# Kernel tuning notes

Hardware: AMD Instinct MI355X
Metric: run time of the kernel (lower is better)

Reference implementation:

```python
import jax, jax.numpy as jnp
import numpy as np

EPS = 1e-5

def setup_inputs() -> dict:
    key = jax.random.key(0)
    ks = jax.random.split(key, 6)
    N, K, Cin, Cout = 40000, 27, 128, 128
    feats = jax.random.normal(ks[0], (N, Cin), dtype=jnp.float32)
    W = jax.random.normal(ks[1], (K, Cin, Cout), dtype=jnp.float32) * (1.0 / np.sqrt(Cin * K))
    gamma = jnp.ones((Cout,), dtype=jnp.float32)
    beta = jnp.zeros((Cout,), dtype=jnp.float32)
    in_idx = jax.random.randint(ks[2], (K, N), 0, N, dtype=jnp.int64)
    out_idx = jax.random.randint(ks[3], (K, N), 0, N, dtype=jnp.int64)
    valid = jax.random.randint(ks[4], (K, N), 0, 2, dtype=jnp.int32)
    return {"feats": feats, "W": W, "gamma": gamma, "beta": beta,
            "in_idx": in_idx, "out_idx": out_idx, "valid": valid}

def reference(feats, W, gamma, beta, in_idx, out_idx, valid) -> jnp.ndarray:
    # Sparse 3D conv as gather-GEMM-scatter over K=27 kernel-offset maps.
    K, M = in_idx.shape
    N = feats.shape[0]  # stride 1 -> N_out == N_in
    mask = (valid > 0).astype(feats.dtype)[..., None]          # [K, M, 1]
    gathered = feats[in_idx] * mask                            # [K, M, Cin]
    msg = jnp.einsum('kmc,kcd->kmd', gathered, W)              # [K, M, Cout]
    out = jax.ops.segment_sum(msg.reshape(K * M, -1),
                              out_idx.reshape(-1),
                              num_segments=N)                   # [N, Cout]
    # MinkowskiBatchNorm (training mode): batch stats over all active points.
    mean = jnp.mean(out, axis=0)
    var = jnp.var(out, axis=0)
    y = (out - mean) * jax.lax.rsqrt(var + EPS) * gamma + beta
    # MinkowskiGELU == exact (erf) GELU.
    return jax.nn.gelu(y, approximate=False)
```

## Files before the change

kernel.cpp:

```cpp
#include <hip/hip_runtime.h>

typedef unsigned short u16;
typedef unsigned int u32;
typedef unsigned long long u64;
using f32x4 = __attribute__((ext_vector_type(4))) float;
using bf16x8 = __attribute__((ext_vector_type(8))) short;

#define CIN 128
#define COUT 128
#define BM 128
#define LDA 136

__device__ inline u16 bf16rn(float f) {
    union { float f; u32 u; } v; v.f = f;
    u32 u = v.u;
    u += 0x7FFFu + ((u >> 16) & 1u);
    return (u16)(u >> 16);
}

__global__ void precast_feats_k(const float* __restrict__ in, u16* __restrict__ out, int total8) {
    int i = blockIdx.x * blockDim.x + threadIdx.x;
    if (i >= total8) return;
    const float4* p = (const float4*)in + 2 * (size_t)i;
    float4 a = p[0], b = p[1];
    u32 o0 = (u32)bf16rn(a.x) | ((u32)bf16rn(a.y) << 16);
    u32 o1 = (u32)bf16rn(a.z) | ((u32)bf16rn(a.w) << 16);
    u32 o2 = (u32)bf16rn(b.x) | ((u32)bf16rn(b.y) << 16);
    u32 o3 = (u32)bf16rn(b.z) | ((u32)bf16rn(b.w) << 16);
    ((uint4*)out)[i] = make_uint4(o0, o1, o2, o3);
}

__global__ void precast_w_k(const float* __restrict__ W, u16* __restrict__ Wt, int total) {
    int i = blockIdx.x * blockDim.x + threadIdx.x;
    if (i >= total) return;
    int k = i >> 14;
    int rem = i & 16383;
    int f = rem >> 9;
    int l = (rem >> 3) & 63;
    int e = rem & 7;
    int cn = f >> 2, kk = f & 3;
    int d = cn * 16 + (l & 15);
    int c = kk * 32 + ((l >> 4) << 3) + e;
    Wt[i] = bf16rn(W[(k << 14) + (c << 7) + d]);
}

__global__ void prep_k(const float* __restrict__ feats, const float* __restrict__ W,
                       const int* __restrict__ oi, const int* __restrict__ valid,
                       u16* __restrict__ fb, u16* __restrict__ Wt,
                       int* __restrict__ cnt, int* __restrict__ pos,
                       int* __restrict__ bc0, int* __restrict__ bc1,
                       int total8, int totalw, int N, int E, int b0, int b1) {
    const int blk = blockIdx.x;
    const int tid = threadIdx.x;
    if (blk < b0) {
        int i = blk * 256 + tid;
        if (i >= total8) return;
        const float4* p = (const float4*)feats + 2 * (size_t)i;
        float4 a = p[0], q = p[1];
        u32 o0 = (u32)bf16rn(a.x) | ((u32)bf16rn(a.y) << 16);
        u32 o1 = (u32)bf16rn(a.z) | ((u32)bf16rn(a.w) << 16);
        u32 o2 = (u32)bf16rn(q.x) | ((u32)bf16rn(q.y) << 16);
        u32 o3 = (u32)bf16rn(q.z) | ((u32)bf16rn(q.w) << 16);
        ((uint4*)fb)[i] = make_uint4(o0, o1, o2, o3);
    } else if (blk < b0 + b1) {
        int i = (blk - b0) * 256 + tid;
        if (i >= totalw) return;
        int k = i >> 14;
        int rem = i & 16383;
        int f = rem >> 9;
        int l = (rem >> 3) & 63;
        int e = rem & 7;
        int cn = f >> 2, kk = f & 3;
        int d = cn * 16 + (l & 15);
        int c = kk * 32 + ((l >> 4) << 3) + e;
        Wt[i] = bf16rn(W[(k << 14) + (c << 7) + d]);
    } else {
        const int b = blk - b0 - b1;
        const int e = b * 256 + tid;
        const int k0 = (b * 256) / N;
        bool v = false; bool g = false;
        if (e < E) {
            v = valid[e] > 0;
            g = (e >= (k0 + 1) * N);
            if (v) pos[e] = atomicAdd(&cnt[oi[e]], 1);
        }
        const int lane = tid & 63, wid = tid >> 6;
        u64 m0 = __ballot(v && !g);
        u64 m1 = __ballot(v && g);
        __shared__ int wt[4][2];
        if (lane == 0) { wt[wid][0] = __popcll(m0); wt[wid][1] = __popcll(m1); }
        __syncthreads();
        if (tid == 0) bc0[b] = wt[0][0] + wt[1][0] + wt[2][0] + wt[3][0];
        if (tid == 1) bc1[b] = wt[0][1] + wt[1][1] + wt[2][1] + wt[3][1];
    }
}

__global__ void hist_k(const int* __restrict__ oi, const int* __restrict__ valid,
                       int* __restrict__ cnt, int* __restrict__ pos,
                       int* __restrict__ bc0, int* __restrict__ bc1, int N, int E) {
    const int tid = threadIdx.x;
    const int b = blockIdx.x;
    const int e = b * 256 + tid;
    const int k0 = (b * 256) / N;
    bool v = false; bool g = false;
    if (e < E) {
        v = valid[e] > 0;
        g = (e >= (k0 + 1) * N);
        if (v) pos[e] = atomicAdd(&cnt[oi[e]], 1);
    }
    const int lane = tid & 63, wid = tid >> 6;
    u64 m0 = __ballot(v && !g);
    u64 m1 = __ballot(v && g);
    __shared__ int wt[4][2];
    if (lane == 0) { wt[wid][0] = __popcll(m0); wt[wid][1] = __popcll(m1); }
    __syncthreads();
    if (tid == 0) bc0[b] = wt[0][0] + wt[1][0] + wt[2][0] + wt[3][0];
    if (tid == 1) bc1[b] = wt[0][1] + wt[1][1] + wt[2][1] + wt[3][1];
}

__global__ void scan_sum_k(const int* __restrict__ cnt, int* __restrict__ bsum, int N) {
    __shared__ int red[256];
    int t = threadIdx.x;
    int i = blockIdx.x * 256 + t;
    red[t] = (i < N) ? cnt[i] : 0;
    __syncthreads();
    #pragma unroll
    for (int d = 128; d > 0; d >>= 1) {
        if (t < d) red[t] += red[t + d];
        __syncthreads();
    }
    if (t == 0) bsum[blockIdx.x] = red[0];
}

__global__ void scan_top_k(int* __restrict__ bsum, int nb) {
    __shared__ int part[1024];
    int t = threadIdx.x;
    int v = (t < nb) ? bsum[t] : 0;
    part[t] = v;
    __syncthreads();
    for (int d = 1; d < 1024; d <<= 1) {
        int x = (t >= d) ? part[t - d] : 0;
        __syncthreads();
        part[t] += x;
        __syncthreads();
    }
    if (t < nb) bsum[t] = part[t] - v;
}

__global__ void scan_apply_kscan_k(const int* __restrict__ cnt, const int* __restrict__ bsum,
                                   int* __restrict__ offs,
                                   const int* __restrict__ bc0, const int* __restrict__ bc1,
                                   int* __restrict__ base0, int* __restrict__ base1,
                                   int* __restrict__ kcount, int N, int nb) {
    const int t = threadIdx.x;
    __shared__ int part[256];
    if ((int)blockIdx.x < nb) {
        int i = blockIdx.x * 256 + t;
        int v = (i < N) ? cnt[i] : 0;
        part[t] = v;
        __syncthreads();
        #pragma unroll
        for (int d = 1; d < 256; d <<= 1) {
            int x = (t >= d) ? part[t - d] : 0;
            __syncthreads();
            part[t] += x;
            __syncthreads();
        }
        int base = bsum[blockIdx.x];
        if (i < N) {
            int excl = base + part[t] - v;
            offs[i] = excl;
            if (i == N - 1) offs[N] = excl + v;
        }
    } else {
        const int k = blockIdx.x - nb;
        const int blo = (k * N) / 256;
        const int bhi = ((k + 1) * N - 1) / 256;
        const int len = bhi - blo + 1;
        const int b = blo + t;
        int k0b = 0, contrib = 0;
        const bool inr = (t < len);
        if (inr) {
            k0b = (b * 256) / N;
            contrib = (k0b == k) ? bc0[b] : bc1[b];
        }
        part[t] = contrib;
        __syncthreads();
        #pragma unroll
        for (int d = 1; d < 256; d <<= 1) {
            int x = (t >= d) ? part[t - d] : 0;
            __syncthreads();
            part[t] += x;
            __syncthreads();
        }
        if (inr) {
            int excl = part[t] - contrib;
            if (k0b == k) base0[b] = excl; else base1[b] = excl;
            if (t == len - 1) kcount[k] = part[t];
        }
    }
}

__global__ void rank_k(const int* __restrict__ oi, const int* __restrict__ ini,
                       const int* __restrict__ valid, const int* __restrict__ pos,
                       const int* __restrict__ offs,
                       const int* __restrict__ base0, const int* __restrict__ base1,
                       int* __restrict__ cin_arr, int* __restrict__ cpos_arr,
                       int N, int E, int cap) {
    const int tid = threadIdx.x;
    const int b = blockIdx.x;
    const int e = b * 256 + tid;
    const int k0 = (b * 256) / N;
    bool v = false; int k = 0, n = 0, ii = 0, p = 0;
    if (e < E) {
        v = valid[e] > 0;
        k = (e >= (k0 + 1) * N) ? k0 + 1 : k0;
        if (v) { n = oi[e]; ii = ini[e]; p = pos[e]; }
    }
    const int g = k - k0;
    const int lane = tid & 63, wid = tid >> 6;
    u64 m0 = __ballot(v && g == 0);
    u64 m1 = __ballot(v && g == 1);
    u64 lt = (1ull << lane) - 1ull;
    int r0 = __popcll(m0 & lt);
    int r1 = __popcll(m1 & lt);
    __shared__ int wt[4][2];
    if (lane == 0) { wt[wid][0] = __popcll(m0); wt[wid][1] = __popcll(m1); }
    __syncthreads();
    if (v) {
        int wbase = 0;
        #pragma unroll
        for (int w2 = 0; w2 < 4; ++w2) if (w2 < wid) wbase += wt[w2][g];
        int kb = g ? base1[b] : base0[b];
        int slot = kb + wbase + (g ? r1 : r0);
        int pg = offs[n] + p;
        cin_arr[k * N + slot] = ii;
        cpos_arr[k * N + slot] = (pg < cap) ? pg : (cap + n);
    }
}

__launch_bounds__(512, 6)
__global__ void convA_k(const u16* __restrict__ fb, const u16* __restrict__ Wt,
                        const int* __restrict__ cin_arr, const int* __restrict__ cpos_arr,
                        const int* __restrict__ kcount, u32* __restrict__ msg,
                        float* __restrict__ out, int N, int cap)
{
    const int k = blockIdx.y;
    const int kc = kcount[k];
    const int m0 = blockIdx.x * BM;
    if (m0 >= kc) return;

    __shared__ __align__(16) u16 Bsub[COUT * CIN];

    const int tid = threadIdx.x;
    const int wave = tid >> 6, lane = tid & 63;
    const int l15 = lane & 15, l4 = lane >> 4;
    const int base = k * N;

    int r0 = m0 + wave * 16 + l15;
    int i0 = cin_arr[base + min(r0, kc - 1)];
    if (r0 >= kc) i0 = 0;
    const u16* pa0 = fb + (size_t)i0 * CIN + l4 * 8;
    bf16x8 a0[4];
    #pragma unroll
    for (int kk = 0; kk < 4; ++kk)
        a0[kk] = *(const bf16x8*)(pa0 + kk * 32);

    {
        const u16* wk = Wt + ((size_t)k << 14);
        #pragma unroll
        for (int j = 0; j < 4; ++j)
            *(uint4*)(Bsub + j * 4096 + tid * 8) = *(const uint4*)(wk + j * 4096 + tid * 8);
    }
    __syncthreads();

    f32x4 acc[8];
    #pragma unroll
    for (int y = 0; y < 8; ++y)
        acc[y] = (f32x4){0.f, 0.f, 0.f, 0.f};

    #pragma unroll
    for (int kk = 0; kk < 4; ++kk) {
        #pragma unroll
        for (int cn = 0; cn < 8; ++cn) {
            bf16x8 b = *(const bf16x8*)(Bsub + (((cn << 2) + kk) << 9) + lane * 8);
            acc[cn] = __builtin_amdgcn_mfma_f32_16x16x32_bf16(a0[kk], b, acc[cn], 0, 0, 0);
        }
    }

    #pragma unroll
    for (int j = 0; j < 4; ++j) {
        int rl = m0 + wave * 16 + l4 * 4 + j;
        if (rl >= kc) continue;
        int v = cpos_arr[base + rl];
        if (v < cap) {
            u32 w0 = (u32)bf16rn(acc[0][j]) | ((u32)bf16rn(acc[1][j]) << 16);
            u32 w1 = (u32)bf16rn(acc[2][j]) | ((u32)bf16rn(acc[3][j]) << 16);
            u32 w2 = (u32)bf16rn(acc[4][j]) | ((u32)bf16rn(acc[5][j]) << 16);
            u32 w3 = (u32)bf16rn(acc[6][j]) | ((u32)bf16rn(acc[7][j]) << 16);
            *(uint4*)(msg + (size_t)v * 64 + 4 * l15) = make_uint4(w0, w1, w2, w3);
        } else {
            int n = v - cap;
            float* dst = out + (size_t)n * COUT + l15;
            #pragma unroll
            for (int cn = 0; cn < 8; ++cn)
                atomicAdd(dst + cn * 16, acc[cn][j]);
        }
    }
}

__global__ void convB_stats_k(const u32* __restrict__ msg, const int* __restrict__ offs,
                              float* __restrict__ out, float* __restrict__ stats,
                              int N, int cap, int nblk)
{
    const int tid = threadIdx.x;
    const int wave = tid >> 6, lane = tid & 63;
    const int sub = lane >> 4, l15 = lane & 15;
    const int colA = l15 + 32 * sub;
    float sA = 0.f, qA = 0.f, sB = 0.f, qB = 0.f;

    for (int n = blockIdx.x * 4 + wave; n < N; n += nblk * 4) {
        int s = min(offs[n], cap), e = min(offs[n + 1], cap);
        float a0 = 0.f, a1 = 0.f, a2 = 0.f, a3 = 0.f;
        float b0 = 0.f, b1 = 0.f, b2 = 0.f, b3 = 0.f;
        for (int r = s; r < e; r += 4) {
            int ent = r + sub;
            uint4 v = make_uint4(0u, 0u, 0u, 0u);
            if (ent < e) v = *(const uint4*)(msg + (size_t)ent * 64 + 4 * l15);
            a0 += __uint_as_float(v.x << 16); b0 += __uint_as_float(v.x & 0xFFFF0000u);
            a1 += __uint_as_float(v.y << 16); b1 += __uint_as_float(v.y & 0xFFFF0000u);
            a2 += __uint_as_float(v.z << 16); b2 += __uint_as_float(v.z & 0xFFFF0000u);
            a3 += __uint_as_float(v.w << 16); b3 += __uint_as_float(v.w & 0xFFFF0000u);
        }
        #define RED4(x) { x += __shfl_xor(x, 16, 64); x += __shfl_xor(x, 32, 64); }
        RED4(a0) RED4(a1) RED4(a2) RED4(a3)
        RED4(b0) RED4(b1) RED4(b2) RED4(b3)
        #undef RED4
        float va = (sub == 0) ? a0 : (sub == 1) ? a1 : (sub == 2) ? a2 : a3;
        float vb = (sub == 0) ? b0 : (sub == 1) ? b1 : (sub == 2) ? b2 : b3;
        float* po = out + (size_t)n * COUT;
        po[colA]      = va;
        po[colA + 16] = vb;
        sA += va; qA += va * va;
        sB += vb; qB += vb * vb;
    }

    __shared__ float st[4][64][4];
    st[wave][lane][0] = sA; st[wave][lane][1] = qA;
    st[wave][lane][2] = sB; st[wave][lane][3] = qB;
    __syncthreads();
    int lane2 = tid >> 2, slot = tid & 3;
    float sum = st[0][lane2][slot] + st[1][lane2][slot]
              + st[2][lane2][slot] + st[3][lane2][slot];
    int colb = (lane2 & 15) + 32 * (lane2 >> 4) + ((slot >= 2) ? 16 : 0);
    atomicAdd(&stats[((slot & 1) ? 128 : 0) + colb], sum);
}

__global__ void convB_k(const u32* __restrict__ msg, const int* __restrict__ offs,
                        float* __restrict__ out, int N, int cap)
{
    int wave = threadIdx.x >> 6, lane = threadIdx.x & 63;
    int n = blockIdx.x * 4 + wave;
    if (n >= N) return;
    int s = min(offs[n], cap), e = min(offs[n + 1], cap);
    float a0 = 0.f, a1 = 0.f;
    int r = s;
    for (; r + 2 <= e; r += 2) {
        u32 v0 = msg[(size_t)r * 64 + lane];
        u32 v1 = msg[(size_t)(r + 1) * 64 + lane];
        a0 += __uint_as_float(v0 << 16) + __uint_as_float(v1 << 16);
        a1 += __uint_as_float(v0 & 0xFFFF0000u) + __uint_as_float(v1 & 0xFFFF0000u);
    }
    if (r < e) {
        u32 v0 = msg[(size_t)r * 64 + lane];
        a0 += __uint_as_float(v0 << 16);
        a1 += __uint_as_float(v0 & 0xFFFF0000u);
    }
    int c0 = (lane >> 2) + ((lane & 3) << 5);
    float* po = out + (size_t)n * COUT;
    po[c0]      += a0;
    po[c0 + 16] += a1;
}

__launch_bounds__(256, 2)
__global__ void conv_k(const u16* __restrict__ fb, const u16* __restrict__ Wt,
                       const int* __restrict__ in_idx, const int* __restrict__ out_idx,
                       const int* __restrict__ valid, float* __restrict__ out, int N)
{
    __shared__ __align__(16) u16 Asub[BM * LDA];
    __shared__ __align__(16) u16 Bsub[COUT * CIN];
    __shared__ int orow[BM];

    const int tile = blockIdx.x;
    const int k = blockIdx.y;
    const int tid = threadIdx.x;
    const int m0 = tile * BM;

    {
        const u16* wk = Wt + ((size_t)k << 14);
        #pragma unroll
        for (int j = 0; j < 8; ++j)
            *(uint4*)(Bsub + j * 2048 + tid * 8) = *(const uint4*)(wk + j * 2048 + tid * 8);
    }
    {
        int r = tid >> 1, half = tid & 1;
        int m = m0 + r;
        int act = 0, ii = 0, oi = -1;
        if (m < N) {
            int base = k * N + m;
            act = valid[base];
            ii  = in_idx[base];
            oi  = out_idx[base];
        }
        if (half == 0) orow[r] = (m < N && act > 0) ? oi : -1;
        if (m < N && act > 0) {
            const u16* src = fb + (size_t)ii * CIN + half * 64;
            u16* dst = Asub + r * LDA + half * 64;
            #pragma unroll
            for (int j = 0; j < 8; ++j)
                *(uint4*)(dst + j * 8) = *(const uint4*)(src + j * 8);
        }
    }
    __syncthreads();

    const int wave = tid >> 6, lane = tid & 63;
    const int l15 = lane & 15, l4 = lane >> 4;

    f32x4 acc[2][8];
    #pragma unroll
    for (int x = 0; x < 2; ++x)
        #pragma unroll
        for (int y = 0; y < 8; ++y)
            acc[x][y] = (f32x4){0.f, 0.f, 0.f, 0.f};

    #pragma unroll
    for (int kk = 0; kk < 4; ++kk) {
        const int coff = kk * 32 + l4 * 8;
        bf16x8 a0 = *(const bf16x8*)(Asub + (wave * 32 + l15) * LDA + coff);
        bf16x8 a1 = *(const bf16x8*)(Asub + (wave * 32 + 16 + l15) * LDA + coff);
        #pragma unroll
        for (int cn = 0; cn < 8; ++cn) {
            bf16x8 b = *(const bf16x8*)(Bsub + (((cn << 2) + kk) << 9) + lane * 8);
            acc[0][cn] = __builtin_amdgcn_mfma_f32_16x16x32_bf16(a0, b, acc[0][cn], 0, 0, 0);
            acc[1][cn] = __builtin_amdgcn_mfma_f32_16x16x32_bf16(a1, b, acc[1][cn], 0, 0, 0);
        }
    }

    #pragma unroll
    for (int rm = 0; rm < 2; ++rm) {
        #pragma unroll
        for (int j = 0; j < 4; ++j) {
            int rl = wave * 32 + rm * 16 + l4 * 4 + j;
            int od = orow[rl];
            if (od >= 0) {
                float* dst = out + (size_t)od * COUT + l15;
                #pragma unroll
                for (int cn = 0; cn < 8; ++cn)
                    atomicAdd(dst + cn * 16, acc[rm][cn][j]);
            }
        }
    }
}

__global__ void stats_k(const float* __restrict__ out, float* __restrict__ stats, int N) {
    const int tid = threadIdx.x;
    const int col = tid & 127;
    const int pr = tid >> 7;
    float s = 0.f, sq = 0.f;
    for (int r = blockIdx.x * 2 + pr; r < N; r += gridDim.x * 2) {
        float v = out[(size_t)r * COUT + col];
        s += v; sq += v * v;
    }
    __shared__ float red[512];
    red[tid] = s;
    red[256 + tid] = sq;
    __syncthreads();
    if (tid < 128) {
        atomicAdd(&stats[col],       red[tid] + red[tid + 128]);
        atomicAdd(&stats[128 + col], red[256 + tid] + red[384 + tid]);
    }
}

__global__ void finalize_k(float* __restrict__ stats, const float* __restrict__ gamma,
                           const float* __restrict__ beta, float invN) {
    int c = threadIdx.x;
    float mean = stats[c] * invN;
    float var = stats[128 + c] * invN - mean * mean;
    float sc = rsqrtf(var + 1e-5f) * gamma[c];
    stats[256 + c] = sc;
    stats[384 + c] = beta[c] - mean * sc;
}

__global__ void bngelu_k(float* __restrict__ out, const float* __restrict__ stats, int total4) {
    int i = blockIdx.x * blockDim.x + threadIdx.x;
    if (i >= total4) return;
    float4 v = ((const float4*)out)[i];
    int cb = (i << 2) & 127;
    float r[4] = {v.x, v.y, v.z, v.w};
    #pragma unroll
    for (int e = 0; e < 4; ++e) {
        int c = cb + e;
        float y = r[e] * stats[256 + c] + stats[384 + c];
        r[e] = 0.5f * y * (1.0f + erff(y * 0.70710678118f));
    }
    ((float4*)out)[i] = make_float4(r[0], r[1], r[2], r[3]);
}

extern "C" void kernel_launch(void* const* d_in, const int* in_sizes, int n_in,
                              void* d_out, int out_size, void* d_ws, size_t ws_size,
                              hipStream_t stream) {
    const float* feats  = (const float*)d_in[0];
    const float* W      = (const float*)d_in[1];
    const float* gamma  = (const float*)d_in[2];
    const float* beta   = (const float*)d_in[3];
    const int*   in_idx = (const int*)d_in[4];
    const int*   outidx = (const int*)d_in[5];
    const int*   valid  = (const int*)d_in[6];
    const int N = in_sizes[0] / CIN;
    const int K = in_sizes[1] / (CIN * COUT);
    const int E = K * N;
    float* out = (float*)d_out;

    const int nb  = (N + 255) / 256;
    const int nbE = (E + 255) / 256;

    const size_t fbB   = ((size_t)N * CIN * 2 + 255) & ~255ull;
    const size_t WtB   = ((size_t)K * CIN * COUT * 2 + 255) & ~255ull;
    const size_t cinB  = ((size_t)E * 4 + 255) & ~255ull;
    const size_t cposB = cinB;
    const size_t posB  = cinB;
    const size_t cntB  = ((size_t)N * 4 + 255) & ~255ull;
    const size_t kcB   = 256;
    const size_t stB   = 2048;
    const size_t offsB = ((size_t)(N + 1) * 4 + 255) & ~255ull;
    const size_t bsB   = ((size_t)nb * 4 + 255) & ~255ull;
    const size_t nbEB  = ((size_t)nbE * 4 + 255) & ~255ull;
    const size_t fixedB = fbB + WtB + cinB + cposB + posB + cntB + kcB + stB + offsB
                        + bsB + 4 * nbEB + 1024;

    int total8 = N * CIN / 8;
    int totalw = K * CIN * COUT;

    if (ws_size >= fixedB + (size_t)1024 * 256 && nb <= 1024 && nb + 1 <= 256) {
        long long capL = ((long long)ws_size - (long long)fixedB) / 256;
        if (capL > (long long)E) capL = E;
        const int cap = (int)capL;
        const int wmode = (cap >= E) ? 1 : 0;

        char* w = (char*)d_ws;
        u32* msg      = (u32*)w;  w += (size_t)cap * 256;
        u16* fb       = (u16*)w;  w += fbB;
        u16* Wt       = (u16*)w;  w += WtB;
        int* cin_arr  = (int*)w;  w += cinB;
        int* cpos_arr = (int*)w;  w += cposB;
        int* pos      = (int*)w;  w += posB;
        int* cnt      = (int*)w;  w += cntB;
        int* kcount   = (int*)w;  w += kcB;
        float* stats  = (float*)w; w += stB;
        int* offs     = (int*)w;  w += offsB;
        int* bsum     = (int*)w;  w += bsB;
        int* bc0      = (int*)w;  w += nbEB;
        int* bc1      = (int*)w;  w += nbEB;
        int* base0    = (int*)w;  w += nbEB;
        int* base1    = (int*)w;

        if (!wmode)
            hipMemsetAsync(out, 0, (size_t)N * COUT * sizeof(float), stream);
        hipMemsetAsync(cnt, 0, cntB + kcB + stB, stream);

        const int b0 = (total8 + 255) / 256;
        const int b1 = (totalw + 255) / 256;
        prep_k<<<b0 + b1 + nbE, 256, 0, stream>>>(feats, W, outidx, valid, fb, Wt,
                                                  cnt, pos, bc0, bc1,
                                                  total8, totalw, N, E, b0, b1);
        scan_sum_k<<<nb, 256, 0, stream>>>(cnt, bsum, N);
        scan_top_k<<<1, 1024, 0, stream>>>(bsum, nb);
        scan_apply_kscan_k<<<nb + K, 256, 0, stream>>>(cnt, bsum, offs, bc0, bc1,
                                                       base0, base1, kcount, N, nb);
        rank_k<<<nbE, 256, 0, stream>>>(outidx, in_idx, valid, pos, offs,
                                        base0, base1, cin_arr, cpos_arr, N, E, cap);

        dim3 gA((N + BM - 1) / BM, K);
        convA_k<<<gA, 512, 0, stream>>>(fb, Wt, cin_arr, cpos_arr, kcount, msg, out, N, cap);

        if (wmode) {
            const int nblk = 2048;
            convB_stats_k<<<nblk, 256, 0, stream>>>(msg, offs, out, stats, N, cap, nblk);
        } else {
            convB_k<<<(N + 3) / 4, 256, 0, stream>>>(msg, offs, out, N, cap);
            stats_k<<<256, 256, 0, stream>>>(out, stats, N);
        }

        finalize_k<<<1, 128, 0, stream>>>(stats, gamma, beta, 1.0f / (float)N);
        bngelu_k<<<(N * COUT / 4 + 255) / 256, 256, 0, stream>>>(out, stats, N * COUT / 4);
    } else {
        u16* fb = (u16*)d_ws;
        u16* Wt = fb + (size_t)N * CIN;
        float* stats = (float*)(Wt + (size_t)K * CIN * COUT);

        hipMemsetAsync(out, 0, (size_t)N * COUT * sizeof(float), stream);
        hipMemsetAsync(stats, 0, 256 * sizeof(float), stream);

        precast_feats_k<<<(total8 + 255) / 256, 256, 0, stream>>>(feats, fb, total8);
        precast_w_k<<<(totalw + 255) / 256, 256, 0, stream>>>(W, Wt, totalw);

        dim3 g((N + BM - 1) / BM, K);
        conv_k<<<g, 256, 0, stream>>>(fb, Wt, in_idx, outidx, valid, out, N);

        stats_k<<<256, 256, 0, stream>>>(out, stats, N);
        finalize_k<<<1, 128, 0, stream>>>(stats, gamma, beta, 1.0f / (float)N);
        bngelu_k<<<(N * COUT / 4 + 255) / 256, 256, 0, stream>>>(out, stats, N * COUT / 4);
    }
}
```

Measured before the change: 174.7 us.

## Make convA persistent per kernel offset with prefetched gather of next chunk

The gather-GEMM kernel now launches a fixed 24 blocks per kernel offset, and each wave loops over 16-row chunks with a stride. The 32 KB weight slice is loaded into shared memory once per block instead of once per 128 rows. The gathered feature rows for the next chunk are loaded while the MFMAs for the current chunk run. In exchange there are fewer blocks in flight (24×27), more registers used for the prefetch buffer, and some risk of load imbalance across waves.

```diff
diff --git a/kernel.cpp b/kernel.cpp
--- a/kernel.cpp
+++ b/kernel.cpp
@@ -243,12 +243,10 @@
 __global__ void convA_k(const u16* __restrict__ fb, const u16* __restrict__ Wt,
                         const int* __restrict__ cin_arr, const int* __restrict__ cpos_arr,
                         const int* __restrict__ kcount, u32* __restrict__ msg,
-                        float* __restrict__ out, int N, int cap)
+                        float* __restrict__ out, int N, int cap, int nbk)
 {
     const int k = blockIdx.y;
     const int kc = kcount[k];
-    const int m0 = blockIdx.x * BM;
-    if (m0 >= kc) return;
 
     __shared__ __align__(16) u16 Bsub[COUT * CIN];
 
@@ -257,15 +255,6 @@
     const int l15 = lane & 15, l4 = lane >> 4;
     const int base = k * N;
 
-    int r0 = m0 + wave * 16 + l15;
-    int i0 = cin_arr[base + min(r0, kc - 1)];
-    if (r0 >= kc) i0 = 0;
-    const u16* pa0 = fb + (size_t)i0 * CIN + l4 * 8;
-    bf16x8 a0[4];
-    #pragma unroll
-    for (int kk = 0; kk < 4; ++kk)
-        a0[kk] = *(const bf16x8*)(pa0 + kk * 32);
-
     {
         const u16* wk = Wt + ((size_t)k << 14);
         #pragma unroll
@@ -274,38 +263,74 @@
     }
     __syncthreads();
 
-    f32x4 acc[8];
-    #pragma unroll
-    for (int y = 0; y < 8; ++y)
-        acc[y] = (f32x4){0.f, 0.f, 0.f, 0.f};
-
-    #pragma unroll
-    for (int kk = 0; kk < 4; ++kk) {
-        #pragma unroll
-        for (int cn = 0; cn < 8; ++cn) {
-            bf16x8 b = *(const bf16x8*)(Bsub + (((cn << 2) + kk) << 9) + lane * 8);
-            acc[cn] = __builtin_amdgcn_mfma_f32_16x16x32_bf16(a0[kk], b, acc[cn], 0, 0, 0);
-        }
-    }
-
-    #pragma unroll
-    for (int j = 0; j < 4; ++j) {
-        int rl = m0 + wave * 16 + l4 * 4 + j;
-        if (rl >= kc) continue;
-        int v = cpos_arr[base + rl];
-        if (v < cap) {
-            u32 w0 = (u32)bf16rn(acc[0][j]) | ((u32)bf16rn(acc[1][j]) << 16);
-            u32 w1 = (u32)bf16rn(acc[2][j]) | ((u32)bf16rn(acc[3][j]) << 16);
-            u32 w2 = (u32)bf16rn(acc[4][j]) | ((u32)bf16rn(acc[5][j]) << 16);
-            u32 w3 = (u32)bf16rn(acc[6][j]) | ((u32)bf16rn(acc[7][j]) << 16);
-            *(uint4*)(msg + (size_t)v * 64 + 4 * l15) = make_uint4(w0, w1, w2, w3);
-        } else {
-            int n = v - cap;
-            float* dst = out + (size_t)n * COUT + l15;
+    const int nch = (kc + 15) >> 4;
+    const int wstep = nbk * 8;
+    int c = blockIdx.x * 8 + wave;
+    if (c >= nch) return;
+
+    bf16x8 a0[4];
+    {
+        int r0 = c * 16 + l15;
+        int i0 = cin_arr[base + min(r0, kc - 1)];
+        if (r0 >= kc) i0 = 0;
+        const u16* pa = fb + (size_t)i0 * CIN + l4 * 8;
+        #pragma unroll
+        for (int kk = 0; kk < 4; ++kk)
+            a0[kk] = *(const bf16x8*)(pa + kk * 32);
+    }
+
+    while (true) {
+        const int cnext = c + wstep;
+        const bool has = (cnext < nch);
+
+        bf16x8 an[4];
+        if (has) {
+            int r1 = cnext * 16 + l15;
+            int i1 = cin_arr[base + min(r1, kc - 1)];
+            if (r1 >= kc) i1 = 0;
+            const u16* pa = fb + (size_t)i1 * CIN + l4 * 8;
             #pragma unroll
-            for (int cn = 0; cn < 8; ++cn)
-                atomicAdd(dst + cn * 16, acc[cn][j]);
-        }
+            for (int kk = 0; kk < 4; ++kk)
+                an[kk] = *(const bf16x8*)(pa + kk * 32);
+        }
+
+        f32x4 acc[8];
+        #pragma unroll
+        for (int y = 0; y < 8; ++y)
+            acc[y] = (f32x4){0.f, 0.f, 0.f, 0.f};
+        #pragma unroll
+        for (int kk = 0; kk < 4; ++kk) {
+            #pragma unroll
+            for (int cn = 0; cn < 8; ++cn) {
+                bf16x8 b = *(const bf16x8*)(Bsub + (((cn << 2) + kk) << 9) + lane * 8);
+                acc[cn] = __builtin_amdgcn_mfma_f32_16x16x32_bf16(a0[kk], b, acc[cn], 0, 0, 0);
+            }
+        }
+
+        #pragma unroll
+        for (int j = 0; j < 4; ++j) {
+            int rl = c * 16 + l4 * 4 + j;
+            if (rl >= kc) continue;
+            int v = cpos_arr[base + rl];
+            if (v < cap) {
+                u32 w0 = (u32)bf16rn(acc[0][j]) | ((u32)bf16rn(acc[1][j]) << 16);
+                u32 w1 = (u32)bf16rn(acc[2][j]) | ((u32)bf16rn(acc[3][j]) << 16);
+                u32 w2 = (u32)bf16rn(acc[4][j]) | ((u32)bf16rn(acc[5][j]) << 16);
+                u32 w3 = (u32)bf16rn(acc[6][j]) | ((u32)bf16rn(acc[7][j]) << 16);
+                *(uint4*)(msg + (size_t)v * 64 + 4 * l15) = make_uint4(w0, w1, w2, w3);
+            } else {
+                int n = v - cap;
+                float* dst = out + (size_t)n * COUT + l15;
+                #pragma unroll
+                for (int cn = 0; cn < 8; ++cn)
+                    atomicAdd(dst + cn * 16, acc[cn][j]);
+            }
+        }
+
+        if (!has) break;
+        #pragma unroll
+        for (int kk = 0; kk < 4; ++kk) a0[kk] = an[kk];
+        c = cnext;
     }
 }
 
@@ -580,8 +605,10 @@
         rank_k<<<nbE, 256, 0, stream>>>(outidx, in_idx, valid, pos, offs,
                                         base0, base1, cin_arr, cpos_arr, N, E, cap);
 
-        dim3 gA((N + BM - 1) / BM, K);
-        convA_k<<<gA, 512, 0, stream>>>(fb, Wt, cin_arr, cpos_arr, kcount, msg, out, N, cap);
+        const int nbk = 24;
+        dim3 gA(nbk, K);
+        convA_k<<<gA, 512, 0, stream>>>(fb, Wt, cin_arr, cpos_arr, kcount, msg, out,
+                                        N, cap, nbk);
 
         if (wmode) {
             const int nblk = 2048;
```

Measured after the change: 429.3 us. 146% more time.
